# Kernel tuning notes

Measured on AMD Instinct MI355X. Metric: run time of the kernel, lower is better.

The kernel has to match this reference:

```python
import jax, jax.numpy as jnp
import numpy as np

N = 100000   # nodes
E = 1600000  # edges (before self-loops)
H = 128      # in_channels == hidden_channels
G = 64       # graphs in batch


def setup_inputs() -> dict:
    key = jax.random.key(0)
    ks = jax.random.split(key, 12)
    s = 1.0 / np.sqrt(H)
    inp = {
        "x": jax.random.normal(ks[0], (N, H), jnp.float32),
        "edge_weight": jax.random.uniform(ks[1], (E,), jnp.float32),
        "edge_index": jax.random.randint(ks[2], (2, E), 0, N, dtype=jnp.int64),
        "batch": jnp.sort(jax.random.randint(ks[3], (N,), 0, G, dtype=jnp.int64)),
        "W1": jax.random.uniform(ks[4], (H, H), jnp.float32, -s, s),
        "b1": jnp.zeros((H,), jnp.float32),
        "W2": jax.random.uniform(ks[5], (H, H), jnp.float32, -s, s),
        "b2": jnp.zeros((H,), jnp.float32),
        "W3": jax.random.uniform(ks[6], (H, H), jnp.float32, -s, s),
        "b3": jnp.zeros((H,), jnp.float32),
        "lin_w": jax.random.uniform(ks[7], (H, 1), jnp.float32, -s, s),
        "lin_b": jax.random.uniform(ks[8], (1,), jnp.float32, -s, s),
    }
    return inp


def reference(x, edge_weight, W1, b1, W2, b2, W3, b3, lin_w, lin_b, edge_index, batch):
    # PyG GCNConv with add_self_loops=True, symmetric normalization.
    loops = jnp.arange(N, dtype=edge_index.dtype)
    row = jnp.concatenate([edge_index[0], loops])  # source
    col = jnp.concatenate([edge_index[1], loops])  # target
    ew = jnp.concatenate([edge_weight, jnp.ones((N,), edge_weight.dtype)])

    deg = jax.ops.segment_sum(ew, col, num_segments=N)          # in-degree (weighted)
    safe = jnp.where(deg > 0, deg, 1.0)
    dinv = jnp.where(deg > 0, jax.lax.rsqrt(safe), 0.0)
    norm = dinv[row] * ew * dinv[col]                            # [E+N]

    def conv(h, W, b):
        h = h @ W                                                # [N,H] dense transform
        msg = h[row] * norm[:, None]                             # gather + scale
        return jax.ops.segment_sum(msg, col, num_segments=N) + b # scatter-add

    h = jax.nn.relu(conv(x, W1, b1))
    h = jax.nn.relu(conv(h, W2, b2))
    h = jax.nn.relu(conv(h, W3, b3))

    # global_mean_pool over graph ids
    sums = jax.ops.segment_sum(h, batch, num_segments=G)         # [G,H]
    cnts = jax.ops.segment_sum(jnp.ones((N,), h.dtype), batch, num_segments=G)
    pooled = sums / jnp.maximum(cnts, 1.0)[:, None]
    # dropout is identity at inference
    return pooled @ lin_w + lin_b                                # [G,1]
```

## Files before the change

kernel.cpp:

```cpp
#include <hip/hip_runtime.h>
#include <stdint.h>

#define N_NODES 100000
#define N_EDGES 1600000
#define HDIM    128
#define G_GRAPHS 64
#define NTOT (N_EDGES + N_NODES)
#define PSLOTS 64
#define NSTRIPS (N_NODES / 16)
#define NTB 1024
#define NDB ((N_EDGES + 2047) / 2048)
#define BSH 9
#define NBK ((N_NODES + 511) / 512)
#define MAXBKT 10240
#define AGRID 2048

static_assert(N_NODES % 16 == 0, "tile/agg");
static_assert(N_NODES < (1 << 17), "src fits 17 bits");

typedef __attribute__((ext_vector_type(8))) short bf16x8;
typedef __attribute__((ext_vector_type(4))) float f32x4;
typedef __attribute__((ext_vector_type(2))) float f32x2;

__device__ __forceinline__ uint32_t f2bf(float x) {
    uint32_t b = __float_as_uint(x);
    return (b + 0x7FFFu + ((b >> 16) & 1u)) >> 16;
}
__device__ __forceinline__ uint32_t pack2(float lo, float hi) {
    return f2bf(lo) | (f2bf(hi) << 16);
}

#define FXSCALE 1099511627776.0f

__global__ void k_wswz(const float* __restrict__ Wa, const float* __restrict__ Wb,
                       const float* __restrict__ Wc, uint16_t* __restrict__ dst) {
    int gi = blockIdx.x * 256 + threadIdx.x;
    int w = gi >> 14, idx = gi & 16383;
    const float* src = (w == 0) ? Wa : (w == 1) ? Wb : Wc;
    int k = idx >> 7, n = idx & 127;
    int kc = k >> 5, kq = (k >> 3) & 3, j = k & 7;
    int nt = n >> 4, nl = n & 15;
    dst[w * 16384 + (((kc * 8 + nt) * 64) + kq * 16 + nl) * 8 + j] = (uint16_t)f2bf(src[idx]);
}

__device__ __forceinline__ bf16x8 load_row_f32(const float* p) {
    float4 a = ((const float4*)p)[0];
    float4 b = ((const float4*)p)[1];
    union { uint32_t u[4]; bf16x8 v; } c;
    c.u[0] = pack2(a.x, a.y); c.u[1] = pack2(a.z, a.w);
    c.u[2] = pack2(b.x, b.y); c.u[3] = pack2(b.z, b.w);
    return c.v;
}

__device__ __forceinline__ void transform_body_l1(int tb, int nTB, int tid,
                                                  const float* __restrict__ hin,
                                                  const bf16x8* __restrict__ Wfrag,
                                                  uint32_t* __restrict__ t) {
    int lane = tid & 63;
    int quad = lane >> 4;
    int mrow = lane & 15;
    int gwave = tb * 4 + (tid >> 6);
    int nwaves = nTB * 4;
    for (int strip = gwave; strip < NSTRIPS; strip += nwaves) {
        const float* hrow = hin + ((size_t)(strip * 16 + mrow)) * 128 + quad * 8;
        bf16x8 A0 = load_row_f32(hrow);
        bf16x8 A1 = load_row_f32(hrow + 32);
        bf16x8 A2 = load_row_f32(hrow + 64);
        bf16x8 A3 = load_row_f32(hrow + 96);
        f32x4 acc[8];
#pragma unroll
        for (int nt = 0; nt < 8; nt++) {
            f32x4 a = {0.f, 0.f, 0.f, 0.f};
            a = __builtin_amdgcn_mfma_f32_16x16x32_bf16(A0, Wfrag[(0 * 8 + nt) * 64 + lane], a, 0, 0, 0);
            a = __builtin_amdgcn_mfma_f32_16x16x32_bf16(A1, Wfrag[(1 * 8 + nt) * 64 + lane], a, 0, 0, 0);
            a = __builtin_amdgcn_mfma_f32_16x16x32_bf16(A2, Wfrag[(2 * 8 + nt) * 64 + lane], a, 0, 0, 0);
            a = __builtin_amdgcn_mfma_f32_16x16x32_bf16(A3, Wfrag[(3 * 8 + nt) * 64 + lane], a, 0, 0, 0);
            acc[nt] = a;
        }
#pragma unroll
        for (int nt = 0; nt < 8; nt++) {
#pragma unroll
            for (int r = 0; r < 4; r++) {
                float v = acc[nt][r];
                float nb = __shfl_xor(v, 1);
                int s16 = __builtin_amdgcn_cvt_pk_fp8_f32(v, nb, 0, false);
                int hi  = __shfl_xor(s16, 2);
                if (!(lane & 3)) {
                    int orow = strip * 16 + quad * 4 + r;
                    int oc = (nt * 16 + mrow) >> 2;
                    t[(size_t)orow * 32 + oc] = (uint32_t)(s16 & 0xffff) | ((uint32_t)hi << 16);
                }
            }
        }
    }
}

__global__ __launch_bounds__(256) void k_tr_count(
        const int* __restrict__ ei, const float* __restrict__ x,
        const bf16x8* __restrict__ Wfrag, uint32_t* __restrict__ t,
        int* __restrict__ partials) {
    __shared__ int hist[NBK];
    int bi = blockIdx.x;
    int q7 = bi / 7, r7 = bi % 7;
    int tq = q7 * 4 + r7;
    bool isT = (r7 < 4) && (tq < NTB);
    int tid = threadIdx.x;
    if (isT) {
        transform_body_l1(tq, NTB, tid, x, Wfrag, t);
    } else {
        int nTbef = q7 * 4 + (r7 < 4 ? r7 : 4);
        if (nTbef > NTB) nTbef = NTB;
        int db = bi - nTbef;
        for (int i = tid; i < NBK; i += 256) hist[i] = 0;
        __syncthreads();
        int e0 = db * 2048 + tid;
#pragma unroll
        for (int k = 0; k < 8; k++) {
            int e = e0 + k * 256;
            if (e < N_EDGES) atomicAdd(&hist[ei[N_EDGES + e] >> BSH], 1);
        }
        __syncthreads();
        for (int i = tid; i < NBK; i += 256) partials[i * NDB + db] = hist[i];
    }
}

__global__ void k_bscan(const int* __restrict__ partials, int* __restrict__ blockBase,
                        int* __restrict__ totals) {
    int b = blockIdx.x, tid = threadIdx.x;
    int v[4]; int s = 0;
#pragma unroll
    for (int j = 0; j < 4; j++) {
        int i = tid * 4 + j;
        v[j] = (i < NDB) ? partials[b * NDB + i] : 0;
        s += v[j];
    }
    __shared__ int sm[256];
    sm[tid] = s; __syncthreads();
    for (int off = 1; off < 256; off <<= 1) {
        int u = 0; if (tid >= off) u = sm[tid - off];
        __syncthreads(); sm[tid] += u; __syncthreads();
    }
    int run = sm[tid] - s;
#pragma unroll
    for (int j = 0; j < 4; j++) {
        int i = tid * 4 + j;
        if (i < NDB) blockBase[b * NDB + i] = run;
        run += v[j];
    }
    if (tid == 255) totals[b] = sm[255];
}

__global__ void k_starts(const int* __restrict__ totals, int* __restrict__ bstart) {
    int tid = threadIdx.x;
    int v = (tid < NBK) ? totals[tid] : 0;
    __shared__ int sm[256];
    sm[tid] = v; __syncthreads();
    for (int off = 1; off < 256; off <<= 1) {
        int u = 0; if (tid >= off) u = sm[tid - off];
        __syncthreads(); sm[tid] += u; __syncthreads();
    }
    if (tid < NBK) bstart[tid] = sm[tid] - v;
    if (tid == 255) bstart[NBK] = sm[255];
}

__global__ __launch_bounds__(256) void k_scatter(
        const int* __restrict__ ei, const float* __restrict__ ew,
        const int* __restrict__ blockBase, const int* __restrict__ bstart,
        uint2* __restrict__ recs) {
    __shared__ int hist[NBK];
    __shared__ int basesh[NBK];
    int tid = threadIdx.x, db = blockIdx.x;
    for (int i = tid; i < NBK; i += 256) {
        hist[i] = 0;
        basesh[i] = bstart[i] + blockBase[i * NDB + db];
    }
    __syncthreads();
    int e0 = db * 2048 + tid;
#pragma unroll
    for (int k = 0; k < 8; k++) {
        int e = e0 + k * 256;
        if (e < N_EDGES) {
            int src = ei[e];
            int dst = ei[N_EDGES + e];
            float w = ew[e];
            int bkt = dst >> BSH;
            int r = atomicAdd(&hist[bkt], 1);
            recs[basesh[bkt] + r] =
                make_uint2((uint32_t)src | ((uint32_t)(dst & 511) << 17),
                           __float_as_uint(w));
        }
    }
}

__global__ __launch_bounds__(256) void k_build(
        const uint2* __restrict__ recs, const int* __restrict__ bstart,
        int* __restrict__ cnt, float* __restrict__ dinv, int* __restrict__ offs,
        int2* __restrict__ csr) {
    __shared__ unsigned long long acc[512];
    __shared__ uint16_t rk[MAXBKT];
    __shared__ int loff[512];
    __shared__ int sm[256];
    int b = blockIdx.x, tid = threadIdx.x;
    int e0 = bstart[b], ne = bstart[b + 1] - e0;
    for (int i = tid; i < 512; i += 256) acc[i] = 0ULL;
    __syncthreads();
    for (int j = tid; j < ne; j += 256) {
        uint2 rc = recs[e0 + j];
        int dl = (rc.x >> 17) & 511;
        float w = __uint_as_float(rc.y);
        unsigned long long pk = (1ULL << 48) | (unsigned long long)(w * FXSCALE);
        unsigned long long old = atomicAdd(&acc[dl], pk);
        rk[j] = (uint16_t)(old >> 48);
    }
    __syncthreads();
    int nb0 = b << BSH;
    int nreal = N_NODES - nb0; if (nreal > 512) nreal = 512;
    int i0 = tid * 2, i1 = tid * 2 + 1;
    int c0 = (i0 < nreal) ? (int)(acc[i0] >> 48) + 1 : 0;
    int c1 = (i1 < nreal) ? (int)(acc[i1] >> 48) + 1 : 0;
    sm[tid] = c0 + c1;
    __syncthreads();
    for (int off = 1; off < 256; off <<= 1) {
        int u = 0; if (tid >= off) u = sm[tid - off];
        __syncthreads(); sm[tid] += u; __syncthreads();
    }
    int run = e0 + nb0 + (sm[tid] - (c0 + c1));
    loff[i0] = run;
    loff[i1] = run + c0;
    if (i0 < nreal) {
        unsigned long long pk = acc[i0];
        int c = (int)(pk >> 48);
        float deg = (float)(pk & ((1ULL << 48) - 1)) * (1.0f / FXSCALE);
        cnt[nb0 + i0] = c;
        offs[nb0 + i0] = run;
        dinv[nb0 + i0] = 1.0f / sqrtf(deg + 1.0f);
        csr[run + c] = make_int2(nb0 + i0, __float_as_int(1.0f));
    }
    if (i1 < nreal) {
        unsigned long long pk = acc[i1];
        int c = (int)(pk >> 48);
        float deg = (float)(pk & ((1ULL << 48) - 1)) * (1.0f / FXSCALE);
        cnt[nb0 + i1] = c;
        offs[nb0 + i1] = run + c0;
        dinv[nb0 + i1] = 1.0f / sqrtf(deg + 1.0f);
        csr[run + c0 + c] = make_int2(nb0 + i1, __float_as_int(1.0f));
    }
    __syncthreads();
    for (int j = tid; j < ne; j += 256) {
        uint2 rc = recs[e0 + j];
        int dl = (rc.x >> 17) & 511;
        int src = rc.x & 0x1ffff;
        csr[loff[dl] + rk[j]] = make_int2(src, (int)rc.y);
    }
}

__global__ void k_norm(int2* __restrict__ csr, const float* __restrict__ dinv) {
    int p = blockIdx.x * 256 + threadIdx.x;
    if (p < NTOT) {
        int2 c = csr[p];
        csr[p].y = __float_as_int(__int_as_float(c.y) * dinv[c.x]);
    }
}

#define FETCH1(j, osrc, wsrc, vv, ww) { \
    int o_ = __builtin_amdgcn_ds_swizzle((int)(osrc), (((j) << 5) | 0x10)); \
    int w_ = __builtin_amdgcn_ds_swizzle((int)(wsrc), (((j) << 5) | 0x10)); \
    ww = __uint_as_float((uint32_t)w_); \
    vv = *(const uint2*)(tb + (uint32_t)o_ + lq8); }
#define FETCH8S(J, osrc, wsrc, va, wa) \
    FETCH1((J) + 0, osrc, wsrc, va[0], wa[0]) \
    FETCH1((J) + 1, osrc, wsrc, va[1], wa[1]) \
    FETCH1((J) + 2, osrc, wsrc, va[2], wa[2]) \
    FETCH1((J) + 3, osrc, wsrc, va[3], wa[3]) \
    FETCH1((J) + 4, osrc, wsrc, va[4], wa[4]) \
    FETCH1((J) + 5, osrc, wsrc, va[5], wa[5]) \
    FETCH1((J) + 6, osrc, wsrc, va[6], wa[6]) \
    FETCH1((J) + 7, osrc, wsrc, va[7], wa[7])

__device__ __forceinline__ void fetch8b(const char* __restrict__ tb, int g4, int lq8,
                                        int base, uint32_t osrc, float wsrc,
                                        uint2 (&va)[8], float (&wf)[8]) {
#pragma unroll
    for (int k = 0; k < 8; k++) {
        int o  = __builtin_amdgcn_ds_bpermute(g4 + base + 4 * k, (int)osrc);
        int wb = __builtin_amdgcn_ds_bpermute(g4 + base + 4 * k, __float_as_int(wsrc));
        wf[k] = __uint_as_float((uint32_t)wb);
        va[k] = *(const uint2*)(tb + (uint32_t)(o + lq8));
    }
}

__device__ __forceinline__ void acc8(const uint2 (&va)[8], const float (&wf)[8],
                                     f32x2& p0, f32x2& p1, f32x2& p2, f32x2& p3) {
#pragma unroll
    for (int k = 0; k < 8; k++) {
        f32x2 lo0 = __builtin_amdgcn_cvt_pk_f32_fp8((int)va[k].x, false);
        f32x2 hi0 = __builtin_amdgcn_cvt_pk_f32_fp8((int)va[k].x, true);
        f32x2 lo1 = __builtin_amdgcn_cvt_pk_f32_fp8((int)va[k].y, false);
        f32x2 hi1 = __builtin_amdgcn_cvt_pk_f32_fp8((int)va[k].y, true);
        f32x2 wp = { wf[k], wf[k] };
        p0 += wp * lo0; p1 += wp * hi0; p2 += wp * lo1; p3 += wp * hi1;
    }
}

__device__ __forceinline__ void aggregate_node(const char* __restrict__ tb,
        const int2* __restrict__ csr, int beg, int num, int ql, int lane, int lq8,
        f32x2& p0, f32x2& p1, f32x2& p2, f32x2& p3) {
    int2 m0 = make_int2(0, 0), m1 = make_int2(0, 0);
    if (ql < num) m0 = csr[beg + ql];
    if (ql + 16 < num) m1 = csr[beg + 16 + ql];
    uint32_t o0 = (uint32_t)m0.x << 7;
    uint32_t o1 = (uint32_t)m1.x << 7;
    bool c1 = num > 8, c2 = num > 16, c3 = num > 24;
    uint2 va[8], vb[8], vc[8], vd[8];
    float wa[8], wb[8], wc[8], wd[8];
    FETCH8S(0, o0, m0.y, va, wa)
    if (c1) { FETCH8S(8, o0, m0.y, vb, wb) }
    if (c2) { FETCH8S(0, o1, m1.y, vc, wc) }
    if (c3) { FETCH8S(8, o1, m1.y, vd, wd) }
    acc8(va, wa, p0, p1, p2, p3);
    if (c1) acc8(vb, wb, p0, p1, p2, p3);
    if (c2) acc8(vc, wc, p0, p1, p2, p3);
    if (c3) acc8(vd, wd, p0, p1, p2, p3);
    if (num > 32) {
        int g4 = (lane & 48) << 2;
        for (int base = 32; base < num; base += 16) {
            int2 mm = make_int2(0, 0);
            if (base + ql < num) mm = csr[beg + base + ql];
            uint32_t oo = (uint32_t)mm.x << 7;
            float mws = __int_as_float(mm.y);
            bool h = base + 8 < num;
            fetch8b(tb, g4, lq8, 0, oo, mws, va, wa);
            if (h) fetch8b(tb, g4, lq8, 32, oo, mws, vb, wb);
            acc8(va, wa, p0, p1, p2, p3);
            if (h) acc8(vb, wb, p0, p1, p2, p3);
        }
    }
}

__device__ __forceinline__ f32x2 relu2(f32x2 p, float dn, f32x2 b) {
    f32x2 r;
    r.x = fmaxf(p.x * dn + b.x, 0.f);
    r.y = fmaxf(p.y * dn + b.y, 0.f);
    return r;
}

__global__ __launch_bounds__(256) void k_agg_tr(
        const uint32_t* __restrict__ tin, const int* __restrict__ offs,
        const int* __restrict__ cnt, const int2* __restrict__ csr,
        const float* __restrict__ dinv, const float* __restrict__ bias,
        const bf16x8* __restrict__ Wfrag, uint32_t* __restrict__ tout) {
    __shared__ uint32_t ht[16 * 16 * 4];
    int tid = threadIdx.x;
    int lane = tid & 63;
    int ql = lane & 15;
    int lq8 = ql << 3;
    int row = (tid >> 6) * 4 + (lane >> 4);
    int quad = lane >> 4;
    int m = lane & 15;
    int wid = tid >> 6;
    for (int strip = blockIdx.x; strip < NSTRIPS; strip += AGRID) {
        int node = strip * 16 + row;
        int beg = offs[node];
        int num = cnt[node] + 1;
        float dn = dinv[node];
        f32x2 p0 = {0.f, 0.f}, p1 = {0.f, 0.f}, p2 = {0.f, 0.f}, p3 = {0.f, 0.f};
        aggregate_node((const char*)tin, csr, beg, num, ql, lane, lq8, p0, p1, p2, p3);
        const f32x2* bp = (const f32x2*)bias;
        p0 = relu2(p0, dn, bp[ql * 4 + 0]);
        p1 = relu2(p1, dn, bp[ql * 4 + 1]);
        p2 = relu2(p2, dn, bp[ql * 4 + 2]);
        p3 = relu2(p3, dn, bp[ql * 4 + 3]);
        {
            int slot = (ql + row) & 15;
            uint32_t* dst = &ht[(row * 16 + slot) * 4];
            dst[0] = pack2(p0.x, p0.y);
            dst[1] = pack2(p1.x, p1.y);
            dst[2] = pack2(p2.x, p2.y);
            dst[3] = pack2(p3.x, p3.y);
        }
        __syncthreads();
        bf16x8 A[4];
#pragma unroll
        for (int c = 0; c < 4; c++) {
            int sl = (c * 4 + quad + m) & 15;
            A[c] = *(const bf16x8*)&ht[(m * 16 + sl) * 4];
        }
        __syncthreads();
#pragma unroll
        for (int u = 0; u < 2; u++) {
            int nt = wid * 2 + u;
            f32x4 a = {0.f, 0.f, 0.f, 0.f};
            a = __builtin_amdgcn_mfma_f32_16x16x32_bf16(A[0], Wfrag[(0 * 8 + nt) * 64 + lane], a, 0, 0, 0);
            a = __builtin_amdgcn_mfma_f32_16x16x32_bf16(A[1], Wfrag[(1 * 8 + nt) * 64 + lane], a, 0, 0, 0);
            a = __builtin_amdgcn_mfma_f32_16x16x32_bf16(A[2], Wfrag[(2 * 8 + nt) * 64 + lane], a, 0, 0, 0);
            a = __builtin_amdgcn_mfma_f32_16x16x32_bf16(A[3], Wfrag[(3 * 8 + nt) * 64 + lane], a, 0, 0, 0);
#pragma unroll
            for (int r = 0; r < 4; r++) {
                float v = a[r];
                float nb = __shfl_xor(v, 1);
                int s16 = __builtin_amdgcn_cvt_pk_fp8_f32(v, nb, 0, false);
                int hi  = __shfl_xor(s16, 2);
                if (!(lane & 3)) {
                    int orow = strip * 16 + quad * 4 + r;
                    int oc = (nt * 16 + m) >> 2;
                    tout[(size_t)orow * 32 + oc] = (uint32_t)(s16 & 0xffff) | ((uint32_t)hi << 16);
                }
            }
        }
    }
}

__global__ __launch_bounds__(256) void k_agg_pool(
        const uint32_t* __restrict__ t, const int* __restrict__ offs,
        const int* __restrict__ cnt, const int2* __restrict__ csr,
        const float* __restrict__ dinv, const float* __restrict__ bias,
        const float* __restrict__ lw, const int* __restrict__ batch,
        float* __restrict__ pp) {
    int tid = threadIdx.x;
    int lane = tid & 63;
    int ql = lane & 15;
    int lq8 = ql << 3;
    for (int strip = blockIdx.x; strip < NSTRIPS; strip += AGRID) {
        int node = strip * 16 + (tid >> 6) * 4 + (lane >> 4);
        int beg = offs[node];
        int num = cnt[node] + 1;
        float dn = dinv[node];
        f32x2 p0 = {0.f, 0.f}, p1 = {0.f, 0.f}, p2 = {0.f, 0.f}, p3 = {0.f, 0.f};
        aggregate_node((const char*)t, csr, beg, num, ql, lane, lq8, p0, p1, p2, p3);
        const f32x2* bp = (const f32x2*)bias;
        p0 = relu2(p0, dn, bp[ql * 4 + 0]);
        p1 = relu2(p1, dn, bp[ql * 4 + 1]);
        p2 = relu2(p2, dn, bp[ql * 4 + 2]);
        p3 = relu2(p3, dn, bp[ql * 4 + 3]);
        const f32x2* wp2 = (const f32x2*)lw;
        f32x2 q0 = wp2[ql * 4 + 0], q1 = wp2[ql * 4 + 1];
        f32x2 q2 = wp2[ql * 4 + 2], q3 = wp2[ql * 4 + 3];
        float d = p0.x * q0.x + p0.y * q0.y + p1.x * q1.x + p1.y * q1.y
                + p2.x * q2.x + p2.y * q2.y + p3.x * q3.x + p3.y * q3.y;
        for (int off = 8; off; off >>= 1) d += __shfl_down(d, off);
        if (ql == 0)
            atomicAdd(&pp[(strip & (PSLOTS - 1)) * G_GRAPHS + batch[node]], d);
    }
}

__global__ void k_final(const float* __restrict__ pp, const int* __restrict__ batch,
                        const float* __restrict__ lb, float* __restrict__ out) {
    int g = threadIdx.x;
    float s = 0.f;
#pragma unroll
    for (int k = 0; k < PSLOTS; k++) s += pp[k * G_GRAPHS + g];
    int lo = 0, hi = N_NODES;
    while (lo < hi) { int m = (lo + hi) >> 1; if (batch[m] < g) lo = m + 1; else hi = m; }
    int beg = lo;
    hi = N_NODES;
    while (lo < hi) { int m = (lo + hi) >> 1; if (batch[m] < g + 1) lo = m + 1; else hi = m; }
    float c = fmaxf((float)(lo - beg), 1.0f);
    out[g] = s / c + lb[0];
}

extern "C" void kernel_launch(void* const* d_in, const int* in_sizes, int n_in,
                              void* d_out, int out_size, void* d_ws, size_t ws_size,
                              hipStream_t stream) {
    const float* x   = (const float*)d_in[0];
    const float* ew  = (const float*)d_in[1];
    const int*   ei  = (const int*)d_in[2];
    const int*   bat = (const int*)d_in[3];
    const float* W1  = (const float*)d_in[4];
    const float* b1  = (const float*)d_in[5];
    const float* W2  = (const float*)d_in[6];
    const float* b2  = (const float*)d_in[7];
    const float* W3  = (const float*)d_in[8];
    const float* b3  = (const float*)d_in[9];
    const float* lw  = (const float*)d_in[10];
    const float* lb  = (const float*)d_in[11];
    float* out = (float*)d_out;

    char* w = (char*)d_ws;
    size_t o = 0;
    auto carve = [&](size_t bytes) -> void* {
        void* p = w + o;
        o = (o + bytes + 255) & ~(size_t)255;
        return p;
    };
    float*    pp     = (float*)carve((size_t)PSLOTS * G_GRAPHS * 4);
    int*      parts  = (int*)  carve((size_t)NBK * NDB * 4);
    int*      bbase  = (int*)  carve((size_t)NBK * NDB * 4);
    int*      totals = (int*)  carve((size_t)NBK * 4);
    int*      bstart = (int*)  carve((size_t)(NBK + 1) * 4);
    uint2*    recs   = (uint2*)carve((size_t)N_EDGES * 8);
    int*      cnt    = (int*)  carve((size_t)N_NODES * 4);
    float*    dinv   = (float*)carve((size_t)N_NODES * 4);
    int*      offs   = (int*)  carve((size_t)N_NODES * 4);
    int2*     csr    = (int2*) carve((size_t)NTOT * 8);
    uint32_t* tA     = (uint32_t*)carve((size_t)N_NODES * 128);
    uint32_t* tB     = (uint32_t*)carve((size_t)N_NODES * 128);
    uint16_t* wsz    = (uint16_t*)carve((size_t)3 * 16384 * 2);
    (void)ws_size; (void)in_sizes; (void)n_in; (void)out_size;

    hipMemsetAsync(pp, 0, (size_t)PSLOTS * G_GRAPHS * 4, stream);

    k_wswz<<<192, 256, 0, stream>>>(W1, W2, W3, wsz);
    k_tr_count<<<NTB + NDB, 256, 0, stream>>>(ei, x, (const bf16x8*)wsz, tA, parts);
    k_bscan<<<NBK, 256, 0, stream>>>(parts, bbase, totals);
    k_starts<<<1, 256, 0, stream>>>(totals, bstart);
    k_scatter<<<NDB, 256, 0, stream>>>(ei, ew, bbase, bstart, recs);
    k_build<<<NBK, 256, 0, stream>>>(recs, bstart, cnt, dinv, offs, csr);
    k_norm<<<(NTOT + 255) / 256, 256, 0, stream>>>(csr, dinv);

    k_agg_tr<<<AGRID, 256, 0, stream>>>(tA, offs, cnt, csr, dinv, b1,
                                        (const bf16x8*)(wsz + 16384), tB);
    k_agg_tr<<<AGRID, 256, 0, stream>>>(tB, offs, cnt, csr, dinv, b2,
                                        (const bf16x8*)(wsz + 2 * 16384), tA);
    k_agg_pool<<<AGRID, 256, 0, stream>>>(tA, offs, cnt, csr, dinv, b3, lw, bat, pp);

    k_final<<<1, G_GRAPHS, 0, stream>>>(pp, bat, lb, out);
}
```

Before: 360.4 us.

## Load CSR edges directly per lane and launch one block per node strip

The aggregation kernels stop loading CSR entries cooperatively and broadcasting them with ds_swizzle/ds_bpermute. Each lane now reads the same 8 edge records directly with uniform addresses and masks out-of-range weights to zero, padding the CSR array with 32 zeroed entries so over-reads stay safe. The grid-stride loop over strips is also replaced by one block per 16-node strip, which removes the loop and one __syncthreads per strip. In exchange every lane issues redundant global/cache loads for the edge records, and many more small blocks are launched.

```diff
diff --git a/kernel.cpp b/kernel.cpp
--- a/kernel.cpp
+++ b/kernel.cpp
@@ -13,7 +13,6 @@
 #define BSH 9
 #define NBK ((N_NODES + 511) / 512)
 #define MAXBKT 10240
-#define AGRID 2048
 
 static_assert(N_NODES % 16 == 0, "tile/agg");
 static_assert(N_NODES < (1 << 17), "src fits 17 bits");
@@ -262,78 +261,50 @@
     }
 }
 
-#define FETCH1(j, osrc, wsrc, vv, ww) { \
-    int o_ = __builtin_amdgcn_ds_swizzle((int)(osrc), (((j) << 5) | 0x10)); \
-    int w_ = __builtin_amdgcn_ds_swizzle((int)(wsrc), (((j) << 5) | 0x10)); \
-    ww = __uint_as_float((uint32_t)w_); \
-    vv = *(const uint2*)(tb + (uint32_t)o_ + lq8); }
-#define FETCH8S(J, osrc, wsrc, va, wa) \
-    FETCH1((J) + 0, osrc, wsrc, va[0], wa[0]) \
-    FETCH1((J) + 1, osrc, wsrc, va[1], wa[1]) \
-    FETCH1((J) + 2, osrc, wsrc, va[2], wa[2]) \
-    FETCH1((J) + 3, osrc, wsrc, va[3], wa[3]) \
-    FETCH1((J) + 4, osrc, wsrc, va[4], wa[4]) \
-    FETCH1((J) + 5, osrc, wsrc, va[5], wa[5]) \
-    FETCH1((J) + 6, osrc, wsrc, va[6], wa[6]) \
-    FETCH1((J) + 7, osrc, wsrc, va[7], wa[7])
-
-__device__ __forceinline__ void fetch8b(const char* __restrict__ tb, int g4, int lq8,
-                                        int base, uint32_t osrc, float wsrc,
-                                        uint2 (&va)[8], float (&wf)[8]) {
+__device__ __forceinline__ void load_e8(const uint2* __restrict__ csr2, int p,
+                                        uint2 (&e)[8]) {
+#pragma unroll
+    for (int k = 0; k < 8; k++) e[k] = csr2[p + k];
+}
+__device__ __forceinline__ void load_r8(const char* __restrict__ tb, int lq8,
+                                        const uint2 (&e)[8], uint2 (&v)[8]) {
+#pragma unroll
+    for (int k = 0; k < 8; k++)
+        v[k] = *(const uint2*)(tb + (((uint32_t)e[k].x << 7) + lq8));
+}
+__device__ __forceinline__ void acc8u(const uint2 (&e)[8], const uint2 (&v)[8],
+                                      int base, int num,
+                                      f32x2& p0, f32x2& p1, f32x2& p2, f32x2& p3) {
 #pragma unroll
     for (int k = 0; k < 8; k++) {
-        int o  = __builtin_amdgcn_ds_bpermute(g4 + base + 4 * k, (int)osrc);
-        int wb = __builtin_amdgcn_ds_bpermute(g4 + base + 4 * k, __float_as_int(wsrc));
-        wf[k] = __uint_as_float((uint32_t)wb);
-        va[k] = *(const uint2*)(tb + (uint32_t)(o + lq8));
-    }
-}
-
-__device__ __forceinline__ void acc8(const uint2 (&va)[8], const float (&wf)[8],
-                                     f32x2& p0, f32x2& p1, f32x2& p2, f32x2& p3) {
-#pragma unroll
-    for (int k = 0; k < 8; k++) {
-        f32x2 lo0 = __builtin_amdgcn_cvt_pk_f32_fp8((int)va[k].x, false);
-        f32x2 hi0 = __builtin_amdgcn_cvt_pk_f32_fp8((int)va[k].x, true);
-        f32x2 lo1 = __builtin_amdgcn_cvt_pk_f32_fp8((int)va[k].y, false);
-        f32x2 hi1 = __builtin_amdgcn_cvt_pk_f32_fp8((int)va[k].y, true);
-        f32x2 wp = { wf[k], wf[k] };
+        float wk = (base + k < num) ? __uint_as_float(e[k].y) : 0.f;
+        f32x2 lo0 = __builtin_amdgcn_cvt_pk_f32_fp8((int)v[k].x, false);
+        f32x2 hi0 = __builtin_amdgcn_cvt_pk_f32_fp8((int)v[k].x, true);
+        f32x2 lo1 = __builtin_amdgcn_cvt_pk_f32_fp8((int)v[k].y, false);
+        f32x2 hi1 = __builtin_amdgcn_cvt_pk_f32_fp8((int)v[k].y, true);
+        f32x2 wp = { wk, wk };
         p0 += wp * lo0; p1 += wp * hi0; p2 += wp * lo1; p3 += wp * hi1;
     }
 }
 
 __device__ __forceinline__ void aggregate_node(const char* __restrict__ tb,
-        const int2* __restrict__ csr, int beg, int num, int ql, int lane, int lq8,
+        const uint2* __restrict__ csr2, int beg, int num, int lq8,
         f32x2& p0, f32x2& p1, f32x2& p2, f32x2& p3) {
-    int2 m0 = make_int2(0, 0), m1 = make_int2(0, 0);
-    if (ql < num) m0 = csr[beg + ql];
-    if (ql + 16 < num) m1 = csr[beg + 16 + ql];
-    uint32_t o0 = (uint32_t)m0.x << 7;
-    uint32_t o1 = (uint32_t)m1.x << 7;
+    uint2 eA[8], eB[8], vA[8], vB[8];
     bool c1 = num > 8, c2 = num > 16, c3 = num > 24;
-    uint2 va[8], vb[8], vc[8], vd[8];
-    float wa[8], wb[8], wc[8], wd[8];
-    FETCH8S(0, o0, m0.y, va, wa)
-    if (c1) { FETCH8S(8, o0, m0.y, vb, wb) }
-    if (c2) { FETCH8S(0, o1, m1.y, vc, wc) }
-    if (c3) { FETCH8S(8, o1, m1.y, vd, wd) }
-    acc8(va, wa, p0, p1, p2, p3);
-    if (c1) acc8(vb, wb, p0, p1, p2, p3);
-    if (c2) acc8(vc, wc, p0, p1, p2, p3);
-    if (c3) acc8(vd, wd, p0, p1, p2, p3);
-    if (num > 32) {
-        int g4 = (lane & 48) << 2;
-        for (int base = 32; base < num; base += 16) {
-            int2 mm = make_int2(0, 0);
-            if (base + ql < num) mm = csr[beg + base + ql];
-            uint32_t oo = (uint32_t)mm.x << 7;
-            float mws = __int_as_float(mm.y);
-            bool h = base + 8 < num;
-            fetch8b(tb, g4, lq8, 0, oo, mws, va, wa);
-            if (h) fetch8b(tb, g4, lq8, 32, oo, mws, vb, wb);
-            acc8(va, wa, p0, p1, p2, p3);
-            if (h) acc8(vb, wb, p0, p1, p2, p3);
-        }
+    load_e8(csr2, beg, eA);
+    load_r8(tb, lq8, eA, vA);
+    if (c1) { load_e8(csr2, beg + 8, eB); load_r8(tb, lq8, eB, vB); }
+    acc8u(eA, vA, 0, num, p0, p1, p2, p3);
+    if (c2) { load_e8(csr2, beg + 16, eA); load_r8(tb, lq8, eA, vA); }
+    if (c1) acc8u(eB, vB, 8, num, p0, p1, p2, p3);
+    if (c3) { load_e8(csr2, beg + 24, eB); load_r8(tb, lq8, eB, vB); }
+    if (c2) acc8u(eA, vA, 16, num, p0, p1, p2, p3);
+    if (c3) acc8u(eB, vB, 24, num, p0, p1, p2, p3);
+    for (int base = 32; base < num; base += 8) {
+        load_e8(csr2, beg + base, eA);
+        load_r8(tb, lq8, eA, vA);
+        acc8u(eA, vA, base, num, p0, p1, p2, p3);
     }
 }
 
@@ -355,56 +326,54 @@
     int ql = lane & 15;
     int lq8 = ql << 3;
     int row = (tid >> 6) * 4 + (lane >> 4);
+    int node = blockIdx.x * 16 + row;
+    int beg = offs[node];
+    int num = cnt[node] + 1;
+    float dn = dinv[node];
+    f32x2 p0 = {0.f, 0.f}, p1 = {0.f, 0.f}, p2 = {0.f, 0.f}, p3 = {0.f, 0.f};
+    aggregate_node((const char*)tin, (const uint2*)csr, beg, num, lq8, p0, p1, p2, p3);
+    const f32x2* bp = (const f32x2*)bias;
+    p0 = relu2(p0, dn, bp[ql * 4 + 0]);
+    p1 = relu2(p1, dn, bp[ql * 4 + 1]);
+    p2 = relu2(p2, dn, bp[ql * 4 + 2]);
+    p3 = relu2(p3, dn, bp[ql * 4 + 3]);
+    {
+        int slot = (ql + row) & 15;
+        uint32_t* dst = &ht[(row * 16 + slot) * 4];
+        dst[0] = pack2(p0.x, p0.y);
+        dst[1] = pack2(p1.x, p1.y);
+        dst[2] = pack2(p2.x, p2.y);
+        dst[3] = pack2(p3.x, p3.y);
+    }
+    __syncthreads();
     int quad = lane >> 4;
     int m = lane & 15;
     int wid = tid >> 6;
-    for (int strip = blockIdx.x; strip < NSTRIPS; strip += AGRID) {
-        int node = strip * 16 + row;
-        int beg = offs[node];
-        int num = cnt[node] + 1;
-        float dn = dinv[node];
-        f32x2 p0 = {0.f, 0.f}, p1 = {0.f, 0.f}, p2 = {0.f, 0.f}, p3 = {0.f, 0.f};
-        aggregate_node((const char*)tin, csr, beg, num, ql, lane, lq8, p0, p1, p2, p3);
-        const f32x2* bp = (const f32x2*)bias;
-        p0 = relu2(p0, dn, bp[ql * 4 + 0]);
-        p1 = relu2(p1, dn, bp[ql * 4 + 1]);
-        p2 = relu2(p2, dn, bp[ql * 4 + 2]);
-        p3 = relu2(p3, dn, bp[ql * 4 + 3]);
-        {
-            int slot = (ql + row) & 15;
-            uint32_t* dst = &ht[(row * 16 + slot) * 4];
-            dst[0] = pack2(p0.x, p0.y);
-            dst[1] = pack2(p1.x, p1.y);
-            dst[2] = pack2(p2.x, p2.y);
-            dst[3] = pack2(p3.x, p3.y);
-        }
-        __syncthreads();
-        bf16x8 A[4];
-#pragma unroll
-        for (int c = 0; c < 4; c++) {
-            int sl = (c * 4 + quad + m) & 15;
-            A[c] = *(const bf16x8*)&ht[(m * 16 + sl) * 4];
-        }
-        __syncthreads();
-#pragma unroll
-        for (int u = 0; u < 2; u++) {
-            int nt = wid * 2 + u;
-            f32x4 a = {0.f, 0.f, 0.f, 0.f};
-            a = __builtin_amdgcn_mfma_f32_16x16x32_bf16(A[0], Wfrag[(0 * 8 + nt) * 64 + lane], a, 0, 0, 0);
-            a = __builtin_amdgcn_mfma_f32_16x16x32_bf16(A[1], Wfrag[(1 * 8 + nt) * 64 + lane], a, 0, 0, 0);
-            a = __builtin_amdgcn_mfma_f32_16x16x32_bf16(A[2], Wfrag[(2 * 8 + nt) * 64 + lane], a, 0, 0, 0);
-            a = __builtin_amdgcn_mfma_f32_16x16x32_bf16(A[3], Wfrag[(3 * 8 + nt) * 64 + lane], a, 0, 0, 0);
-#pragma unroll
-            for (int r = 0; r < 4; r++) {
-                float v = a[r];
-                float nb = __shfl_xor(v, 1);
-                int s16 = __builtin_amdgcn_cvt_pk_fp8_f32(v, nb, 0, false);
-                int hi  = __shfl_xor(s16, 2);
-                if (!(lane & 3)) {
-                    int orow = strip * 16 + quad * 4 + r;
-                    int oc = (nt * 16 + m) >> 2;
-                    tout[(size_t)orow * 32 + oc] = (uint32_t)(s16 & 0xffff) | ((uint32_t)hi << 16);
-                }
+    bf16x8 A[4];
+#pragma unroll
+    for (int c = 0; c < 4; c++) {
+        int sl = (c * 4 + quad + m) & 15;
+        A[c] = *(const bf16x8*)&ht[(m * 16 + sl) * 4];
+    }
+    int strip = blockIdx.x;
+#pragma unroll
+    for (int u = 0; u < 2; u++) {
+        int nt = wid * 2 + u;
+        f32x4 a = {0.f, 0.f, 0.f, 0.f};
+        a = __builtin_amdgcn_mfma_f32_16x16x32_bf16(A[0], Wfrag[(0 * 8 + nt) * 64 + lane], a, 0, 0, 0);
+        a = __builtin_amdgcn_mfma_f32_16x16x32_bf16(A[1], Wfrag[(1 * 8 + nt) * 64 + lane], a, 0, 0, 0);
+        a = __builtin_amdgcn_mfma_f32_16x16x32_bf16(A[2], Wfrag[(2 * 8 + nt) * 64 + lane], a, 0, 0, 0);
+        a = __builtin_amdgcn_mfma_f32_16x16x32_bf16(A[3], Wfrag[(3 * 8 + nt) * 64 + lane], a, 0, 0, 0);
+#pragma unroll
+        for (int r = 0; r < 4; r++) {
+            float v = a[r];
+            float nb = __shfl_xor(v, 1);
+            int s16 = __builtin_amdgcn_cvt_pk_fp8_f32(v, nb, 0, false);
+            int hi  = __shfl_xor(s16, 2);
+            if (!(lane & 3)) {
+                int orow = strip * 16 + quad * 4 + r;
+                int oc = (nt * 16 + m) >> 2;
+                tout[(size_t)orow * 32 + oc] = (uint32_t)(s16 & 0xffff) | ((uint32_t)hi << 16);
             }
         }
     }
@@ -420,27 +389,25 @@
     int lane = tid & 63;
     int ql = lane & 15;
     int lq8 = ql << 3;
-    for (int strip = blockIdx.x; strip < NSTRIPS; strip += AGRID) {
-        int node = strip * 16 + (tid >> 6) * 4 + (lane >> 4);
-        int beg = offs[node];
-        int num = cnt[node] + 1;
-        float dn = dinv[node];
-        f32x2 p0 = {0.f, 0.f}, p1 = {0.f, 0.f}, p2 = {0.f, 0.f}, p3 = {0.f, 0.f};
-        aggregate_node((const char*)t, csr, beg, num, ql, lane, lq8, p0, p1, p2, p3);
-        const f32x2* bp = (const f32x2*)bias;
-        p0 = relu2(p0, dn, bp[ql * 4 + 0]);
-        p1 = relu2(p1, dn, bp[ql * 4 + 1]);
-        p2 = relu2(p2, dn, bp[ql * 4 + 2]);
-        p3 = relu2(p3, dn, bp[ql * 4 + 3]);
-        const f32x2* wp2 = (const f32x2*)lw;
-        f32x2 q0 = wp2[ql * 4 + 0], q1 = wp2[ql * 4 + 1];
-        f32x2 q2 = wp2[ql * 4 + 2], q3 = wp2[ql * 4 + 3];
-        float d = p0.x * q0.x + p0.y * q0.y + p1.x * q1.x + p1.y * q1.y
-                + p2.x * q2.x + p2.y * q2.y + p3.x * q3.x + p3.y * q3.y;
-        for (int off = 8; off; off >>= 1) d += __shfl_down(d, off);
-        if (ql == 0)
-            atomicAdd(&pp[(strip & (PSLOTS - 1)) * G_GRAPHS + batch[node]], d);
-    }
+    int node = blockIdx.x * 16 + (tid >> 6) * 4 + (lane >> 4);
+    int beg = offs[node];
+    int num = cnt[node] + 1;
+    float dn = dinv[node];
+    f32x2 p0 = {0.f, 0.f}, p1 = {0.f, 0.f}, p2 = {0.f, 0.f}, p3 = {0.f, 0.f};
+    aggregate_node((const char*)t, (const uint2*)csr, beg, num, lq8, p0, p1, p2, p3);
+    const f32x2* bp = (const f32x2*)bias;
+    p0 = relu2(p0, dn, bp[ql * 4 + 0]);
+    p1 = relu2(p1, dn, bp[ql * 4 + 1]);
+    p2 = relu2(p2, dn, bp[ql * 4 + 2]);
+    p3 = relu2(p3, dn, bp[ql * 4 + 3]);
+    const f32x2* wp2 = (const f32x2*)lw;
+    f32x2 q0 = wp2[ql * 4 + 0], q1 = wp2[ql * 4 + 1];
+    f32x2 q2 = wp2[ql * 4 + 2], q3 = wp2[ql * 4 + 3];
+    float d = p0.x * q0.x + p0.y * q0.y + p1.x * q1.x + p1.y * q1.y
+            + p2.x * q2.x + p2.y * q2.y + p3.x * q3.x + p3.y * q3.y;
+    for (int off = 8; off; off >>= 1) d += __shfl_down(d, off);
+    if (ql == 0)
+        atomicAdd(&pp[(blockIdx.x & (PSLOTS - 1)) * G_GRAPHS + batch[node]], d);
 }
 
 __global__ void k_final(const float* __restrict__ pp, const int* __restrict__ batch,
@@ -491,13 +458,14 @@
     int*      cnt    = (int*)  carve((size_t)N_NODES * 4);
     float*    dinv   = (float*)carve((size_t)N_NODES * 4);
     int*      offs   = (int*)  carve((size_t)N_NODES * 4);
-    int2*     csr    = (int2*) carve((size_t)NTOT * 8);
+    int2*     csr    = (int2*) carve((size_t)(NTOT + 32) * 8);
     uint32_t* tA     = (uint32_t*)carve((size_t)N_NODES * 128);
     uint32_t* tB     = (uint32_t*)carve((size_t)N_NODES * 128);
     uint16_t* wsz    = (uint16_t*)carve((size_t)3 * 16384 * 2);
     (void)ws_size; (void)in_sizes; (void)n_in; (void)out_size;
 
     hipMemsetAsync(pp, 0, (size_t)PSLOTS * G_GRAPHS * 4, stream);
+    hipMemsetAsync(csr + NTOT, 0, 32 * sizeof(int2), stream);
 
     k_wswz<<<192, 256, 0, stream>>>(W1, W2, W3, wsz);
     k_tr_count<<<NTB + NDB, 256, 0, stream>>>(ei, x, (const bf16x8*)wsz, tA, parts);
@@ -507,11 +475,11 @@
     k_build<<<NBK, 256, 0, stream>>>(recs, bstart, cnt, dinv, offs, csr);
     k_norm<<<(NTOT + 255) / 256, 256, 0, stream>>>(csr, dinv);
 
-    k_agg_tr<<<AGRID, 256, 0, stream>>>(tA, offs, cnt, csr, dinv, b1,
-                                        (const bf16x8*)(wsz + 16384), tB);
-    k_agg_tr<<<AGRID, 256, 0, stream>>>(tB, offs, cnt, csr, dinv, b2,
-                                        (const bf16x8*)(wsz + 2 * 16384), tA);
-    k_agg_pool<<<AGRID, 256, 0, stream>>>(tA, offs, cnt, csr, dinv, b3, lw, bat, pp);
+    k_agg_tr<<<NSTRIPS, 256, 0, stream>>>(tA, offs, cnt, csr, dinv, b1,
+                                          (const bf16x8*)(wsz + 16384), tB);
+    k_agg_tr<<<NSTRIPS, 256, 0, stream>>>(tB, offs, cnt, csr, dinv, b2,
+                                          (const bf16x8*)(wsz + 2 * 16384), tA);
+    k_agg_pool<<<NSTRIPS, 256, 0, stream>>>(tA, offs, cnt, csr, dinv, b3, lw, bat, pp);
 
     k_final<<<1, G_GRAPHS, 0, stream>>>(pp, bat, lb, out);
 }
```

Result: faster. 343.5 us (-4.7%).
